# Optimization experiments

Measured on AMD Instinct MI355X. Metric: run time of the kernel, lower is better.

The kernel has to match this reference:

```python
import jax, jax.numpy as jnp
import numpy as np

C_IN = 512
C = 64        # per-head dim
N_HEAD = 8
B, S = 2, 2048


def setup_inputs() -> dict:
    key = jax.random.key(0)
    ks = jax.random.split(key, 9)
    scale = 1.0 / np.sqrt(C_IN)
    return {
        "x": jax.random.normal(ks[0], (B, S, C_IN), dtype=jnp.float32),
        "bias": jax.random.normal(ks[1], (B, N_HEAD, S, S), dtype=jnp.float32),
        "Wq": jax.random.normal(ks[2], (N_HEAD * C, C_IN), dtype=jnp.float32) * scale,
        "Wk": jax.random.normal(ks[3], (N_HEAD * C, C_IN), dtype=jnp.float32) * scale,
        "Wv": jax.random.normal(ks[4], (N_HEAD * C, C_IN), dtype=jnp.float32) * scale,
        "Wo": jax.random.normal(ks[5], (C_IN, N_HEAD * C), dtype=jnp.float32) * scale,
        "bo": jax.random.normal(ks[6], (C_IN,), dtype=jnp.float32) * 0.01,
        "Wg": jax.random.normal(ks[7], (N_HEAD * C, C_IN), dtype=jnp.float32) * scale,
        "bg": jax.random.normal(ks[8], (N_HEAD * C,), dtype=jnp.float32) * 0.01,
    }


def reference(x, bias, Wq, Wk, Wv, Wo, bo, Wg, bg):
    # x: [B, S, C_IN]; attn_dim=1 -> q/k/v axis is already at -2 after movedim.
    # Project and split heads: [B, S, H*C] -> [B, H, S, C]
    def split_heads(t):
        Bq, Sq, _ = t.shape
        return t.reshape(Bq, Sq, N_HEAD, C).transpose(0, 2, 1, 3)

    q = split_heads(x @ Wq.T) / jnp.sqrt(jnp.asarray(C, x.dtype))
    k = split_heads(x @ Wk.T)
    v = split_heads(x @ Wv.T)

    a = jnp.einsum("bhqc,bhkc->bhqk", q, k) + bias   # [B, H, S, S]
    a = jax.nn.softmax(a, axis=-1)
    o = jnp.einsum("bhqk,bhkc->bhqc", a, v)          # [B, H, S, C]

    # merge heads back: [B, S, H*C]
    o = o.transpose(0, 2, 1, 3).reshape(x.shape[0], x.shape[1], N_HEAD * C)
    g = jax.nn.sigmoid(x @ Wg.T + bg)
    o = g * o
    return o @ Wo.T + bo                              # [B, S, C_IN]
```

## Files before the change

kernel.cpp:

```cpp
#include <hip/hip_runtime.h>
#include <math.h>

#define BB 2
#define HH 8
#define SS 2048
#define CC 64
#define CIN 512
#define DDIM 512
#define MM (BB*SS)
#define NCHUNK (SS / 64)

#define LOG2E 1.4426950408889634f
#define SHIFT2 (16.0f * LOG2E)

using short8  = __attribute__((ext_vector_type(8))) short;
using float4v = __attribute__((ext_vector_type(4))) float;

__device__ __forceinline__ unsigned short tob(float f) {
    unsigned u = __float_as_uint(f);
    unsigned r = (u + 0x7fffu + ((u >> 16) & 1u)) >> 16;
    return (unsigned short)r;
}
__device__ __forceinline__ float fromb(unsigned short u) {
    return __uint_as_float(((unsigned)u) << 16);
}

#define GLDS(srcp, ldsp)                                                     \
    __builtin_amdgcn_global_load_lds(                                        \
        (const __attribute__((address_space(1))) void*)(srcp),               \
        (__attribute__((address_space(3))) void*)(ldsp), 16, 0, 0)

__global__ __launch_bounds__(256) void convert_all(
    const float* __restrict__ x,
    const float* __restrict__ wq, const float* __restrict__ wk,
    const float* __restrict__ wv, const float* __restrict__ wg,
    const float* __restrict__ wo,
    unsigned short* __restrict__ xb,
    unsigned short* __restrict__ wqb, unsigned short* __restrict__ wkb,
    unsigned short* __restrict__ wvb, unsigned short* __restrict__ wgb,
    unsigned short* __restrict__ wob)
{
    const int NX4 = MM * CIN / 4;
    int i = blockIdx.x * blockDim.x + threadIdx.x;
    const float* src; unsigned short* dst; float scale = 1.0f; int off;
    if (i < NX4) { src = x; dst = xb; off = i; }
    else {
        int j = i - NX4;
        int seg = j >> 16;
        off = j & 65535;
        if      (seg == 0) { src = wq; dst = wqb; scale = 0.125f * LOG2E; }
        else if (seg == 1) { src = wk; dst = wkb; }
        else if (seg == 2) { src = wv; dst = wvb; }
        else if (seg == 3) { src = wg; dst = wgb; }
        else               { src = wo; dst = wob; }
    }
    float4 v = ((const float4*)src)[off];
    ushort4 o;
    o.x = tob(v.x * scale); o.y = tob(v.y * scale);
    o.z = tob(v.z * scale); o.w = tob(v.w * scale);
    ((ushort4*)dst)[off] = o;
}

__global__ __launch_bounds__(256) void proj_gemm(
    const unsigned short* __restrict__ X,
    const unsigned short* __restrict__ Wq,
    const unsigned short* __restrict__ Wk,
    const unsigned short* __restrict__ Wv,
    const unsigned short* __restrict__ Wg,
    const float* __restrict__ bg,
    unsigned short* __restrict__ Qd,
    unsigned short* __restrict__ Kd,
    unsigned short* __restrict__ Vd,
    unsigned short* __restrict__ Gd)
{
    __shared__ __align__(16) unsigned short At[64][72];
    __shared__ __align__(16) unsigned short Bt[64][72];

    int mode = blockIdx.z;
    const unsigned short* W = (mode == 0) ? Wq : (mode == 1) ? Wk : (mode == 2) ? Wv : Wg;

    int m0 = blockIdx.y * 64;
    int n0 = blockIdx.x * 64;
    int tid = threadIdx.x;
    int w = tid >> 6, lane = tid & 63;
    int quad = lane >> 4, l16 = lane & 15;
    int wm = w & 1, wn = w >> 1;

    float4v acc[2][2];
    for (int a = 0; a < 2; ++a) for (int c = 0; c < 2; ++c) acc[a][c] = (float4v)0.0f;

    for (int kc = 0; kc < CIN; kc += 64) {
        for (int it = 0; it < 2; ++it) {
            int idx = it * 2048 + tid * 8;
            int row = idx >> 6, col = idx & 63;
            *(short8*)&At[row][col] = *(const short8*)&X[(size_t)(m0 + row) * CIN + kc + col];
            *(short8*)&Bt[row][col] = *(const short8*)&W[(size_t)(n0 + row) * CIN + kc + col];
        }
        __syncthreads();
        for (int ks = 0; ks < 2; ++ks) {
            short8 a0 = *(const short8*)&At[wm * 32 + l16][ks * 32 + quad * 8];
            short8 a1 = *(const short8*)&At[wm * 32 + 16 + l16][ks * 32 + quad * 8];
            short8 b0 = *(const short8*)&Bt[wn * 32 + l16][ks * 32 + quad * 8];
            short8 b1 = *(const short8*)&Bt[wn * 32 + 16 + l16][ks * 32 + quad * 8];
            acc[0][0] = __builtin_amdgcn_mfma_f32_16x16x32_bf16(a0, b0, acc[0][0], 0, 0, 0);
            acc[0][1] = __builtin_amdgcn_mfma_f32_16x16x32_bf16(a0, b1, acc[0][1], 0, 0, 0);
            acc[1][0] = __builtin_amdgcn_mfma_f32_16x16x32_bf16(a1, b0, acc[1][0], 0, 0, 0);
            acc[1][1] = __builtin_amdgcn_mfma_f32_16x16x32_bf16(a1, b1, acc[1][1], 0, 0, 0);
        }
        __syncthreads();
    }

    if (mode == 2) {
        for (int a = 0; a < 2; ++a) for (int c = 0; c < 2; ++c)
            for (int r = 0; r < 4; ++r) {
                int ml = wm * 32 + a * 16 + quad * 4 + r;
                int nl = wn * 32 + c * 16 + l16;
                At[nl][ml] = tob(acc[a][c][r]);
            }
        __syncthreads();
        int bi = m0 >> 11, h = n0 >> 6, s0 = m0 & 2047;
        int crow = tid >> 2, seg = tid & 3;
        unsigned short* dp = Vd + (((size_t)(bi * HH + h) * CC) + crow) * SS + s0 + seg * 16;
        *(short8*)dp       = *(const short8*)&At[crow][seg * 16];
        *(short8*)(dp + 8) = *(const short8*)&At[crow][seg * 16 + 8];
        return;
    }

    for (int a = 0; a < 2; ++a) for (int c = 0; c < 2; ++c)
        for (int r = 0; r < 4; ++r) {
            int gm = m0 + wm * 32 + a * 16 + quad * 4 + r;
            int gn = n0 + wn * 32 + c * 16 + l16;
            float v = acc[a][c][r];
            if (mode <= 1) {
                int bi = gm >> 11, s = gm & 2047, h = gn >> 6, cc = gn & 63;
                unsigned short* d = (mode == 0) ? Qd : Kd;
                d[(((size_t)(bi * HH + h) * SS) + s) * CC + cc] = tob(v);
            } else {
                float g = 1.0f / (1.0f + __expf(-(v + bg[gn])));
                Gd[(size_t)gm * DDIM + gn] = tob(g);
            }
        }
}

__global__ __launch_bounds__(256, 2) void attn_kernel(
    const unsigned short* __restrict__ Q,
    const unsigned short* __restrict__ K,
    const unsigned short* __restrict__ V,
    const float* __restrict__ bias,
    const unsigned short* __restrict__ G,
    unsigned short* __restrict__ Om)
{
    __shared__ __align__(16) unsigned short Kt[2][64][64];
    __shared__ __align__(16) unsigned short Vt[2][64][64];
    __shared__ __align__(16) float Bs[2][64][64];
    __shared__ __align__(16) unsigned short Pt[4][16][72];

    int qb = blockIdx.x * 64;
    int bh = blockIdx.y;
    int b = bh >> 3, h = bh & 7;
    int tid = threadIdx.x;
    int w = tid >> 6, lane = tid & 63;
    int quad = lane >> 4, l16 = lane & 15;
    int swl = l16 & 7;

    int phase = (blockIdx.x + blockIdx.y) & (NCHUNK - 1);

    const unsigned short* Qbh = Q + (size_t)bh * SS * CC;
    const unsigned short* Kbh = K + (size_t)bh * SS * CC;
    const unsigned short* Vbh = V + (size_t)bh * CC * SS;
    const float* Bbh = bias + (size_t)bh * SS * SS;

    int qrow = qb + w * 16 + l16;
    short8 aq0 = *(const short8*)&Qbh[(size_t)qrow * CC + quad * 8];
    short8 aq1 = *(const short8*)&Qbh[(size_t)qrow * CC + 32 + quad * 8];

    float lsum[4] = {0.f, 0.f, 0.f, 0.f};
    float4v accO[4];
    for (int jn = 0; jn < 4; ++jn) accO[jn] = (float4v)0.0f;

    int row8  = lane >> 3;
    int kswz  = (lane & 7) ^ row8;
    int row16 = lane >> 4;
    int col16 = lane & 15;

    auto STAGE = [&](int d, int kb) {
#pragma unroll
        for (int p = 0; p < 2; ++p) {
            int r0 = w * 16 + p * 8;
            GLDS(Kbh + (size_t)(kb + r0 + row8) * CC + kswz * 8, &Kt[d][r0][0]);
            GLDS(Vbh + (size_t)(r0 + row8) * SS + kb + kswz * 8, &Vt[d][r0][0]);
        }
#pragma unroll
        for (int t = 0; t < 4; ++t) {
            int r0 = w * 16 + t * 4;
            GLDS(Bbh + (size_t)(qb + r0 + row16) * SS + kb + col16 * 4, &Bs[d][r0][0]);
        }
    };

    STAGE(0, phase * 64);
    STAGE(1, ((1 + phase) & (NCHUNK - 1)) * 64);

    for (int c = 0; c < NCHUNK; ++c) {
        int d = c & 1;
        if (c + 1 < NCHUNK) {
            asm volatile("s_waitcnt vmcnt(8)" ::: "memory");
        } else {
            asm volatile("s_waitcnt vmcnt(0)" ::: "memory");
        }
        __builtin_amdgcn_sched_barrier(0);
        __builtin_amdgcn_s_barrier();
        __builtin_amdgcn_sched_barrier(0);

        float4v sa[4];
#pragma unroll
        for (int j = 0; j < 4; ++j) sa[j] = (float4v)(-SHIFT2);
#pragma unroll
        for (int j = 0; j < 4; ++j) {
            short8 bk0 = *(const short8*)&Kt[d][j * 16 + l16][((quad    ) ^ swl) * 8];
            short8 bk1 = *(const short8*)&Kt[d][j * 16 + l16][((quad + 4) ^ swl) * 8];
            sa[j] = __builtin_amdgcn_mfma_f32_16x16x32_bf16(aq0, bk0, sa[j], 0, 0, 0);
            sa[j] = __builtin_amdgcn_mfma_f32_16x16x32_bf16(aq1, bk1, sa[j], 0, 0, 0);
        }

#pragma unroll
        for (int j = 0; j < 4; ++j)
#pragma unroll
            for (int r = 0; r < 4; ++r) {
                float bb = Bs[d][w * 16 + quad * 4 + r][j * 16 + l16];
                float p = __builtin_amdgcn_exp2f(fmaf(bb, LOG2E, sa[j][r]));
                lsum[r] += p;
                Pt[w][quad * 4 + r][j * 16 + l16] = tob(p);
            }

#pragma unroll
        for (int ks = 0; ks < 2; ++ks) {
            short8 ap = *(const short8*)&Pt[w][l16][ks * 32 + quad * 8];
#pragma unroll
            for (int jn = 0; jn < 4; ++jn) {
                short8 bv = *(const short8*)&Vt[d][jn * 16 + l16][((ks * 4 + quad) ^ swl) * 8];
                accO[jn] = __builtin_amdgcn_mfma_f32_16x16x32_bf16(ap, bv, accO[jn], 0, 0, 0);
            }
        }

        __builtin_amdgcn_sched_barrier(0);
        asm volatile("s_waitcnt lgkmcnt(0)" ::: "memory");
        __builtin_amdgcn_s_barrier();
        __builtin_amdgcn_sched_barrier(0);

        if (c + 2 < NCHUNK)
            STAGE(d, ((c + 2 + phase) & (NCHUNK - 1)) * 64);
    }

    float rl[4];
#pragma unroll
    for (int r = 0; r < 4; ++r) {
        float s = lsum[r];
        s += __shfl_xor(s, 1, 64);
        s += __shfl_xor(s, 2, 64);
        s += __shfl_xor(s, 4, 64);
        s += __shfl_xor(s, 8, 64);
        rl[r] = 1.0f / s;
    }

    int mrow = b * SS + qb + w * 16 + quad * 4;
#pragma unroll
    for (int jn = 0; jn < 4; ++jn)
#pragma unroll
        for (int r = 0; r < 4; ++r) {
            int col = h * 64 + jn * 16 + l16;
            float g = fromb(G[(size_t)(mrow + r) * DDIM + col]);
            Om[(size_t)(mrow + r) * DDIM + col] = tob(accO[jn][r] * rl[r] * g);
        }
}

__global__ __launch_bounds__(256) void out_gemm(
    const unsigned short* __restrict__ Og,
    const unsigned short* __restrict__ W,
    const float* __restrict__ bo,
    float* __restrict__ out)
{
    __shared__ __align__(16) unsigned short At[64][72];
    __shared__ __align__(16) unsigned short Bt[64][72];

    int m0 = blockIdx.y * 64;
    int n0 = blockIdx.x * 64;
    int tid = threadIdx.x;
    int w = tid >> 6, lane = tid & 63;
    int quad = lane >> 4, l16 = lane & 15;
    int wm = w & 1, wn = w >> 1;

    float4v acc[2][2];
    for (int a = 0; a < 2; ++a) for (int c = 0; c < 2; ++c) acc[a][c] = (float4v)0.0f;

    for (int kc = 0; kc < DDIM; kc += 64) {
        for (int it = 0; it < 2; ++it) {
            int idx = it * 2048 + tid * 8;
            int row = idx >> 6, col = idx & 63;
            *(short8*)&At[row][col] = *(const short8*)&Og[(size_t)(m0 + row) * DDIM + kc + col];
            *(short8*)&Bt[row][col] = *(const short8*)&W[(size_t)(n0 + row) * DDIM + kc + col];
        }
        __syncthreads();
        for (int ks = 0; ks < 2; ++ks) {
            short8 a0 = *(const short8*)&At[wm * 32 + l16][ks * 32 + quad * 8];
            short8 a1 = *(const short8*)&At[wm * 32 + 16 + l16][ks * 32 + quad * 8];
            short8 b0 = *(const short8*)&Bt[wn * 32 + l16][ks * 32 + quad * 8];
            short8 b1 = *(const short8*)&Bt[wn * 32 + 16 + l16][ks * 32 + quad * 8];
            acc[0][0] = __builtin_amdgcn_mfma_f32_16x16x32_bf16(a0, b0, acc[0][0], 0, 0, 0);
            acc[0][1] = __builtin_amdgcn_mfma_f32_16x16x32_bf16(a0, b1, acc[0][1], 0, 0, 0);
            acc[1][0] = __builtin_amdgcn_mfma_f32_16x16x32_bf16(a1, b0, acc[1][0], 0, 0, 0);
            acc[1][1] = __builtin_amdgcn_mfma_f32_16x16x32_bf16(a1, b1, acc[1][1], 0, 0, 0);
        }
        __syncthreads();
    }

    for (int a = 0; a < 2; ++a) for (int c = 0; c < 2; ++c)
        for (int r = 0; r < 4; ++r) {
            int gm = m0 + wm * 32 + a * 16 + quad * 4 + r;
            int gn = n0 + wn * 32 + c * 16 + l16;
            out[(size_t)gm * DDIM + gn] = acc[a][c][r] + bo[gn];
        }
}

extern "C" void kernel_launch(void* const* d_in, const int* in_sizes, int n_in,
                              void* d_out, int out_size, void* d_ws, size_t ws_size,
                              hipStream_t stream)
{
    const float* x    = (const float*)d_in[0];
    const float* bias = (const float*)d_in[1];
    const float* Wq   = (const float*)d_in[2];
    const float* Wk   = (const float*)d_in[3];
    const float* Wv   = (const float*)d_in[4];
    const float* Wo   = (const float*)d_in[5];
    const float* bo   = (const float*)d_in[6];
    const float* Wg   = (const float*)d_in[7];
    const float* bg   = (const float*)d_in[8];
    float* out = (float*)d_out;

    char* ws = (char*)d_ws;
    auto alloc = [&](size_t bytes) { char* p = ws; ws += (bytes + 255) & ~(size_t)255; return p; };
    unsigned short* xb  = (unsigned short*)alloc((size_t)MM * CIN * 2);
    unsigned short* wqb = (unsigned short*)alloc((size_t)DDIM * CIN * 2);
    unsigned short* wkb = (unsigned short*)alloc((size_t)DDIM * CIN * 2);
    unsigned short* wvb = (unsigned short*)alloc((size_t)DDIM * CIN * 2);
    unsigned short* wgb = (unsigned short*)alloc((size_t)DDIM * CIN * 2);
    unsigned short* wob = (unsigned short*)alloc((size_t)DDIM * CIN * 2);
    unsigned short* Qh  = (unsigned short*)alloc((size_t)BB * HH * SS * CC * 2);
    unsigned short* Kh  = (unsigned short*)alloc((size_t)BB * HH * SS * CC * 2);
    unsigned short* Vh  = (unsigned short*)alloc((size_t)BB * HH * SS * CC * 2);
    unsigned short* Gt  = (unsigned short*)alloc((size_t)MM * DDIM * 2);
    unsigned short* Om  = (unsigned short*)alloc((size_t)MM * DDIM * 2);

    convert_all<<<3328, 256, 0, stream>>>(x, Wq, Wk, Wv, Wg, Wo,
                                          xb, wqb, wkb, wvb, wgb, wob);
    proj_gemm<<<dim3(DDIM / 64, MM / 64, 4), 256, 0, stream>>>(
        xb, wqb, wkb, wvb, wgb, bg, Qh, Kh, Vh, Gt);
    attn_kernel<<<dim3(SS / 64, BB * HH), 256, 0, stream>>>(
        Qh, Kh, Vh, bias, Gt, Om);
    out_gemm<<<dim3(DDIM / 64, MM / 64), 256, 0, stream>>>(Om, wob, bo, out);
}
```

Measured before the change: 450.1 us.

## Shrink attention key chunk to 32 and use 4-deep LDS ring buffer

The attention kernel now streams K/V/bias in 32-key chunks through a 4-buffer LDS ring with prefetch distance 3, instead of 64-key chunks double-buffered. The staging for chunk c+3 is issued right after the top-of-loop barrier, which removes the second per-iteration barrier. The goal is to keep more loads in flight and hide global latency with less synchronisation. In exchange there are twice as many iterations, each with less MFMA work, and a new V swizzle pattern that must line up with the read side.

```diff
diff --git a/kernel.cpp b/kernel.cpp
--- a/kernel.cpp
+++ b/kernel.cpp
@@ -8,7 +8,9 @@
 #define CIN 512
 #define DDIM 512
 #define MM (BB*SS)
-#define NCHUNK (SS / 64)
+#define KCHUNK 32
+#define NCHUNK (SS / KCHUNK)
+#define NBUF 4
 
 #define LOG2E 1.4426950408889634f
 #define SHIFT2 (16.0f * LOG2E)
@@ -150,10 +152,10 @@
     const unsigned short* __restrict__ G,
     unsigned short* __restrict__ Om)
 {
-    __shared__ __align__(16) unsigned short Kt[2][64][64];
-    __shared__ __align__(16) unsigned short Vt[2][64][64];
-    __shared__ __align__(16) float Bs[2][64][64];
-    __shared__ __align__(16) unsigned short Pt[4][16][72];
+    __shared__ __align__(16) unsigned short Kt[NBUF][32][64];
+    __shared__ __align__(16) unsigned short Vt[NBUF][64][32];
+    __shared__ __align__(16) float Bs[NBUF][64][32];
+    __shared__ __align__(16) unsigned short Pt[4][16][40];
 
     int qb = blockIdx.x * 64;
     int bh = blockIdx.y;
@@ -162,6 +164,7 @@
     int w = tid >> 6, lane = tid & 63;
     int quad = lane >> 4, l16 = lane & 15;
     int swl = l16 & 7;
+    int vsw = l16 & 3;
 
     int phase = (blockIdx.x + blockIdx.y) & (NCHUNK - 1);
 
@@ -178,32 +181,32 @@
     float4v accO[4];
     for (int jn = 0; jn < 4; ++jn) accO[jn] = (float4v)0.0f;
 
-    int row8  = lane >> 3;
-    int kswz  = (lane & 7) ^ row8;
-    int row16 = lane >> 4;
-    int col16 = lane & 15;
+    int row8 = lane >> 3;
+    int kswz = (lane & 7) ^ row8;
+    int row4 = lane >> 2;
+    int vswz = (lane & 3) ^ (row4 & 3);
 
     auto STAGE = [&](int d, int kb) {
-#pragma unroll
-        for (int p = 0; p < 2; ++p) {
-            int r0 = w * 16 + p * 8;
-            GLDS(Kbh + (size_t)(kb + r0 + row8) * CC + kswz * 8, &Kt[d][r0][0]);
-            GLDS(Vbh + (size_t)(r0 + row8) * SS + kb + kswz * 8, &Vt[d][r0][0]);
-        }
-#pragma unroll
-        for (int t = 0; t < 4; ++t) {
-            int r0 = w * 16 + t * 4;
-            GLDS(Bbh + (size_t)(qb + r0 + row16) * SS + kb + col16 * 4, &Bs[d][r0][0]);
-        }
+        GLDS(Kbh + (size_t)(kb + w * 8 + row8) * CC + kswz * 8, &Kt[d][w * 8][0]);
+        GLDS(Vbh + (size_t)(w * 16 + row4) * SS + kb + vswz * 8, &Vt[d][w * 16][0]);
+#pragma unroll
+        for (int t = 0; t < 2; ++t)
+            GLDS(Bbh + (size_t)(qb + w * 16 + t * 8 + row8) * SS + kb + (lane & 7) * 4,
+                 &Bs[d][w * 16 + t * 8][0]);
     };
 
-    STAGE(0, phase * 64);
-    STAGE(1, ((1 + phase) & (NCHUNK - 1)) * 64);
-
+    STAGE(0, ((0 + phase) & (NCHUNK - 1)) * KCHUNK);
+    STAGE(1, ((1 + phase) & (NCHUNK - 1)) * KCHUNK);
+    STAGE(2, ((2 + phase) & (NCHUNK - 1)) * KCHUNK);
+
+#pragma unroll 4
     for (int c = 0; c < NCHUNK; ++c) {
-        int d = c & 1;
-        if (c + 1 < NCHUNK) {
+        int d = c & (NBUF - 1);
+        __builtin_amdgcn_sched_barrier(0);
+        if (c + 2 < NCHUNK) {
             asm volatile("s_waitcnt vmcnt(8)" ::: "memory");
+        } else if (c + 1 < NCHUNK) {
+            asm volatile("s_waitcnt vmcnt(4)" ::: "memory");
         } else {
             asm volatile("s_waitcnt vmcnt(0)" ::: "memory");
         }
@@ -211,11 +214,14 @@
         __builtin_amdgcn_s_barrier();
         __builtin_amdgcn_sched_barrier(0);
 
-        float4v sa[4];
-#pragma unroll
-        for (int j = 0; j < 4; ++j) sa[j] = (float4v)(-SHIFT2);
-#pragma unroll
-        for (int j = 0; j < 4; ++j) {
+        if (c + 3 < NCHUNK)
+            STAGE((c + 3) & (NBUF - 1), ((c + 3 + phase) & (NCHUNK - 1)) * KCHUNK);
+
+        float4v sa[2];
+#pragma unroll
+        for (int j = 0; j < 2; ++j) sa[j] = (float4v)(-SHIFT2);
+#pragma unroll
+        for (int j = 0; j < 2; ++j) {
             short8 bk0 = *(const short8*)&Kt[d][j * 16 + l16][((quad    ) ^ swl) * 8];
             short8 bk1 = *(const short8*)&Kt[d][j * 16 + l16][((quad + 4) ^ swl) * 8];
             sa[j] = __builtin_amdgcn_mfma_f32_16x16x32_bf16(aq0, bk0, sa[j], 0, 0, 0);
@@ -223,7 +229,7 @@
         }
 
 #pragma unroll
-        for (int j = 0; j < 4; ++j)
+        for (int j = 0; j < 2; ++j)
 #pragma unroll
             for (int r = 0; r < 4; ++r) {
                 float bb = Bs[d][w * 16 + quad * 4 + r][j * 16 + l16];
@@ -232,23 +238,18 @@
                 Pt[w][quad * 4 + r][j * 16 + l16] = tob(p);
             }
 
-#pragma unroll
-        for (int ks = 0; ks < 2; ++ks) {
-            short8 ap = *(const short8*)&Pt[w][l16][ks * 32 + quad * 8];
+        {
+            short8 ap = *(const short8*)&Pt[w][l16][quad * 8];
 #pragma unroll
             for (int jn = 0; jn < 4; ++jn) {
-                short8 bv = *(const short8*)&Vt[d][jn * 16 + l16][((ks * 4 + quad) ^ swl) * 8];
+                short8 bv = *(const short8*)&Vt[d][jn * 16 + l16][(quad ^ vsw) * 8];
                 accO[jn] = __builtin_amdgcn_mfma_f32_16x16x32_bf16(ap, bv, accO[jn], 0, 0, 0);
             }
         }
 
         __builtin_amdgcn_sched_barrier(0);
         asm volatile("s_waitcnt lgkmcnt(0)" ::: "memory");
-        __builtin_amdgcn_s_barrier();
-        __builtin_amdgcn_sched_barrier(0);
-
-        if (c + 2 < NCHUNK)
-            STAGE(d, ((c + 2 + phase) & (NCHUNK - 1)) * 64);
+        __builtin_amdgcn_sched_barrier(0);
     }
 
     float rl[4];
```

Result: slower. 463.9 us (+3.1%).
